# Kernel optimization log

Measured on AMD Instinct MI355X. Metric: run time of the kernel, lower is better.

## Reference

```python
import jax, jax.numpy as jnp
import numpy as np

DIM = 4096
N_HEADS = 32
HEAD_DIM = DIM // N_HEADS  # 128
BSZ = 2
SEQLEN = 2048


def setup_inputs() -> dict:
    key = jax.random.key(0)
    ks = jax.random.split(key, 8)
    x = jax.random.normal(ks[0], (BSZ, SEQLEN, DIM), dtype=jnp.float32)
    # rotary frequencies (LLaMA): theta = 10000^{-2i/d}, angle = pos * theta
    inv_freq = 1.0 / (10000.0 ** (np.arange(0, HEAD_DIM, 2, dtype=np.float32) / HEAD_DIM))
    angles = np.arange(SEQLEN, dtype=np.float32)[:, None] * inv_freq[None, :]  # [S, hd/2]
    freqs_cos = jnp.asarray(np.cos(angles))
    freqs_sin = jnp.asarray(np.sin(angles))
    # causal additive mask [1,1,S,S]
    neg = jnp.float32(-1e9)
    mask = jnp.where(jnp.tril(jnp.ones((SEQLEN, SEQLEN), dtype=bool)), 0.0, neg)[None, None]
    scale = 0.02
    wq = jax.random.normal(ks[1], (DIM, DIM), dtype=jnp.float32) * scale
    wk = jax.random.normal(ks[2], (DIM, DIM), dtype=jnp.float32) * scale
    wv = jax.random.normal(ks[3], (DIM, DIM), dtype=jnp.float32) * scale
    wo = jax.random.normal(ks[4], (DIM, DIM), dtype=jnp.float32) * scale
    return {"x": x, "start_pos": 0, "freqs_cos": freqs_cos, "freqs_sin": freqs_sin,
            "mask": mask, "wq": wq, "wk": wk, "wv": wv, "wo": wo}


def _apply_rotary(t, cos, sin):
    # t: [B,S,H,hd]; cos/sin: [S,hd/2] -> broadcast [1,S,1,hd/2]
    t = t.reshape(*t.shape[:-1], HEAD_DIM // 2, 2)
    t0, t1 = t[..., 0], t[..., 1]
    c = cos[None, :, None, :]
    s = sin[None, :, None, :]
    r0 = t0 * c - t1 * s
    r1 = t0 * s + t1 * c
    return jnp.stack([r0, r1], axis=-1).reshape(*t0.shape[:-1], HEAD_DIM)


def reference(x, start_pos, freqs_cos, freqs_sin, mask, wq, wk, wv, wo):
    bsz, seqlen, _ = x.shape
    # QKV projections (nn.Linear: y = x @ W.T; weights stored [out,in])
    xq = (x @ wq.T).reshape(bsz, seqlen, N_HEADS, HEAD_DIM)
    xk = (x @ wk.T).reshape(bsz, seqlen, N_HEADS, HEAD_DIM)
    xv = (x @ wv.T).reshape(bsz, seqlen, N_HEADS, HEAD_DIM)
    xq = _apply_rotary(xq, freqs_cos, freqs_sin)
    xk = _apply_rotary(xk, freqs_cos, freqs_sin)
    # [B,H,S,hd]
    q = xq.transpose(0, 2, 1, 3)
    k = xk.transpose(0, 2, 1, 3)
    v = xv.transpose(0, 2, 1, 3)
    scale = 1.0 / jnp.sqrt(jnp.float32(HEAD_DIM))
    scores = jnp.einsum('bhqd,bhkd->bhqk', q, k) * scale + mask
    probs = jax.nn.softmax(scores, axis=-1)
    out = jnp.einsum('bhqk,bhkd->bhqd', probs, v)  # [B,H,S,hd]
    out = out.transpose(0, 2, 1, 3).reshape(bsz, seqlen, DIM)
    return out @ wo.T
```

## Files before the change

kernel.cpp:

```cpp
#include <hip/hip_runtime.h>

typedef unsigned short ushort_t;
typedef unsigned int u32;
typedef short bf16x8 __attribute__((ext_vector_type(8)));
typedef float f32x4 __attribute__((ext_vector_type(4)));
typedef float f32x16 __attribute__((ext_vector_type(16)));
typedef u32 u32x4 __attribute__((ext_vector_type(4)));

__device__ __forceinline__ ushort_t f2bf(float f) {
  u32 u = __builtin_bit_cast(u32, f);
  u += 0x7FFFu + ((u >> 16) & 1u);
  return (ushort_t)(u >> 16);
}
__device__ __forceinline__ float bf2f(u32 bits16) {
  return __builtin_bit_cast(float, bits16 << 16);
}

__global__ __launch_bounds__(256)
void cvt_kernel(const float* __restrict__ in, ushort_t* __restrict__ out) {
  const int i = blockIdx.x * 256 + threadIdx.x;
  const float4 a = ((const float4*)in)[(size_t)i * 2];
  const float4 b = ((const float4*)in)[(size_t)i * 2 + 1];
  uint4 r;
  r.x = (u32)f2bf(a.x) | ((u32)f2bf(a.y) << 16);
  r.y = (u32)f2bf(a.z) | ((u32)f2bf(a.w) << 16);
  r.z = (u32)f2bf(b.x) | ((u32)f2bf(b.y) << 16);
  r.w = (u32)f2bf(b.z) | ((u32)f2bf(b.w) << 16);
  ((uint4*)out)[i] = r;
}

template <int F32OUT>
__global__ __launch_bounds__(512, 2)
void gemm256(const ushort_t* __restrict__ A, const ushort_t* __restrict__ B,
             void* __restrict__ C) {
  constexpr int KD = 4096, ND = 4096;
  __shared__ ushort_t sA[2][2][128 * 64];
  __shared__ ushort_t sB[2][2][128 * 64];
  const int tid = threadIdx.x;
  const int lane = tid & 63, wave = tid >> 6;
  const int lq = lane & 15, g = lane >> 4;
  const int wm = wave >> 2, wn = wave & 3;
  const int id = blockIdx.x;
  const int swz = (id & 7) * 32 + (id >> 3);
  const int bm = (swz >> 4) * 256;
  const int bn = (swz & 15) * 256;
  const int csw = ((lane & 7) ^ (lane >> 3)) * 8;
  const int srow = lane >> 3;

  f32x4 acc[8][4];
#pragma unroll
  for (int m = 0; m < 8; ++m)
#pragma unroll
    for (int n = 0; n < 4; ++n) acc[m][n] = (f32x4)0.f;

#define STG(sbuf, G, rowb, t_, s_, h_)                                               \
  {                                                                                  \
    _Pragma("unroll") for (int i_ = 0; i_ < 2; ++i_) {                               \
      const int r0_ = wave * 16 + i_ * 8;                                            \
      const int tc_ = (t_) > 63 ? 63 : (t_);                                         \
      const ushort_t* src_ =                                                         \
          (G) + (size_t)((rowb) + (h_) * 128 + r0_ + srow) * KD + tc_ * 64 + csw;    \
      __builtin_amdgcn_global_load_lds(                                              \
          (const __attribute__((address_space(1))) u32*)src_,                        \
          (__attribute__((address_space(3))) u32*)&sbuf[s_][h_][r0_ * 64 + lane * 8],\
          16, 0, 0);                                                                 \
    }                                                                                \
  }
#define LGKM0                                          \
  asm volatile("s_waitcnt lgkmcnt(0)" ::: "memory");   \
  __builtin_amdgcn_sched_barrier(0)

  STG(sA, A, bm, 0, 0, 0); STG(sA, A, bm, 0, 0, 1);
  STG(sB, B, bn, 0, 0, 0); STG(sB, B, bn, 0, 0, 1);
  asm volatile("s_waitcnt vmcnt(4)" ::: "memory");
  STG(sA, A, bm, 1, 1, 0); STG(sA, A, bm, 1, 1, 1);
  STG(sB, B, bn, 1, 1, 1);
  asm volatile("s_waitcnt vmcnt(6)" ::: "memory");
  __builtin_amdgcn_s_barrier();

  bf16x8 af[4][2], b0[2][2], b1[2][2];

  for (int t = 0; t < 64; ++t) {
    const int s = t & 1;
#pragma unroll
    for (int mf = 0; mf < 4; ++mf)
#pragma unroll
      for (int kk = 0; kk < 2; ++kk)
        af[mf][kk] = *(const bf16x8*)
            &sA[s][0][(wm * 64 + mf * 16 + lq) * 64 + (((kk * 4 + g) ^ (lq & 7)) * 8)];
#pragma unroll
    for (int nf = 0; nf < 2; ++nf)
#pragma unroll
      for (int kk = 0; kk < 2; ++kk)
        b0[nf][kk] = *(const bf16x8*)
            &sB[s][0][(wn * 32 + nf * 16 + lq) * 64 + (((kk * 4 + g) ^ (lq & 7)) * 8)];
    STG(sB, B, bn, t + 1, s ^ 1, 0);
    __builtin_amdgcn_s_barrier();
    LGKM0;
    __builtin_amdgcn_s_setprio(1);
#pragma unroll
    for (int mf = 0; mf < 4; ++mf)
#pragma unroll
      for (int nf = 0; nf < 2; ++nf)
#pragma unroll
        for (int kk = 0; kk < 2; ++kk)
          acc[mf][nf] = __builtin_amdgcn_mfma_f32_16x16x32_bf16(af[mf][kk], b0[nf][kk],
                                                                acc[mf][nf], 0, 0, 0);
    __builtin_amdgcn_s_setprio(0);
    __builtin_amdgcn_s_barrier();
#pragma unroll
    for (int nf = 0; nf < 2; ++nf)
#pragma unroll
      for (int kk = 0; kk < 2; ++kk)
        b1[nf][kk] = *(const bf16x8*)
            &sB[s][1][(wn * 32 + nf * 16 + lq) * 64 + (((kk * 4 + g) ^ (lq & 7)) * 8)];
    __builtin_amdgcn_s_barrier();
    LGKM0;
    __builtin_amdgcn_s_setprio(1);
#pragma unroll
    for (int mf = 0; mf < 4; ++mf)
#pragma unroll
      for (int nf = 0; nf < 2; ++nf)
#pragma unroll
        for (int kk = 0; kk < 2; ++kk)
          acc[mf][2 + nf] = __builtin_amdgcn_mfma_f32_16x16x32_bf16(af[mf][kk], b1[nf][kk],
                                                                    acc[mf][2 + nf], 0, 0, 0);
    __builtin_amdgcn_s_setprio(0);
    __builtin_amdgcn_s_barrier();
#pragma unroll
    for (int mf = 0; mf < 4; ++mf)
#pragma unroll
      for (int kk = 0; kk < 2; ++kk)
        af[mf][kk] = *(const bf16x8*)
            &sA[s][1][(wm * 64 + mf * 16 + lq) * 64 + (((kk * 4 + g) ^ (lq & 7)) * 8)];
    STG(sA, A, bm, t + 2, s, 0);
    __builtin_amdgcn_s_barrier();
    LGKM0;
    __builtin_amdgcn_s_setprio(1);
#pragma unroll
    for (int mf = 0; mf < 4; ++mf)
#pragma unroll
      for (int nf = 0; nf < 2; ++nf)
#pragma unroll
        for (int kk = 0; kk < 2; ++kk)
          acc[4 + mf][2 + nf] = __builtin_amdgcn_mfma_f32_16x16x32_bf16(
              af[mf][kk], b1[nf][kk], acc[4 + mf][2 + nf], 0, 0, 0);
    __builtin_amdgcn_s_setprio(0);
    __builtin_amdgcn_s_barrier();
    STG(sA, A, bm, t + 2, s, 1);
    STG(sB, B, bn, t + 2, s, 1);
    __builtin_amdgcn_s_barrier();
    __builtin_amdgcn_s_setprio(1);
#pragma unroll
    for (int mf = 0; mf < 4; ++mf)
#pragma unroll
      for (int nf = 0; nf < 2; ++nf)
#pragma unroll
        for (int kk = 0; kk < 2; ++kk)
          acc[4 + mf][nf] = __builtin_amdgcn_mfma_f32_16x16x32_bf16(
              af[mf][kk], b0[nf][kk], acc[4 + mf][nf], 0, 0, 0);
    __builtin_amdgcn_s_setprio(0);
    asm volatile("s_waitcnt vmcnt(6)" ::: "memory");
    __builtin_amdgcn_s_barrier();
  }
#undef STG
#undef LGKM0

#pragma unroll
  for (int m = 0; m < 8; ++m) {
    const int grow = bm + (m >> 2) * 128 + wm * 64 + (m & 3) * 16 + g * 4;
#pragma unroll
    for (int r = 0; r < 4; ++r)
#pragma unroll
      for (int n = 0; n < 4; ++n) {
        const int gcol = bn + (n >> 1) * 128 + wn * 32 + (n & 1) * 16 + lq;
        if (F32OUT)
          ((float*)C)[(size_t)(grow + r) * ND + gcol] = acc[m][n][r];
        else
          ((ushort_t*)C)[(size_t)(grow + r) * ND + gcol] = f2bf(acc[m][n][r]);
      }
  }
}

__global__ __launch_bounds__(256)
void rope_kernel(ushort_t* __restrict__ Q, ushort_t* __restrict__ K,
                 const float* __restrict__ fcos, const float* __restrict__ fsin) {
  const int gid = blockIdx.x * 256 + threadIdx.x;
  ushort_t* T = blockIdx.y ? K : Q;
  const float scale = blockIdx.y ? 1.f : 0.08838834764831845f;
  const int j8 = gid & 15;
  const int h = (gid >> 4) & 31;
  const int s = (gid >> 9) & 2047;
  const int b = gid >> 20;
  const size_t off = (size_t)(b * 2048 + s) * 4096 + h * 128 + j8 * 8;
  uint4 v = *(const uint4*)(T + off);
  const float4 c4 = *(const float4*)(fcos + s * 64 + j8 * 4);
  const float4 s4 = *(const float4*)(fsin + s * 64 + j8 * 4);
  u32 w[4] = {v.x, v.y, v.z, v.w};
  const float cc[4] = {c4.x, c4.y, c4.z, c4.w};
  const float ss[4] = {s4.x, s4.y, s4.z, s4.w};
#pragma unroll
  for (int p = 0; p < 4; ++p) {
    const float t0 = bf2f(w[p] & 0xffffu);
    const float t1 = bf2f(w[p] >> 16);
    const float r0 = (t0 * cc[p] - t1 * ss[p]) * scale;
    const float r1 = (t0 * ss[p] + t1 * cc[p]) * scale;
    w[p] = (u32)f2bf(r0) | ((u32)f2bf(r1) << 16);
  }
  v.x = w[0]; v.y = w[1]; v.z = w[2]; v.w = w[3];
  *(uint4*)(T + off) = v;
}

__global__ __launch_bounds__(256, 2)
void attn_kernel(const ushort_t* __restrict__ Q, const ushort_t* __restrict__ K,
                 const ushort_t* __restrict__ Vt, ushort_t* __restrict__ O) {
  __shared__ ushort_t sK[2][32 * 128];
  __shared__ ushort_t sV[2][128 * 32];
  __shared__ float sScr[4][32];

  const int lane = threadIdx.x & 63, wave = threadIdx.x >> 6;
  const int lq = lane & 31, hi = lane >> 5;
  const int bp = blockIdx.x;
  const int bh = bp >> 3, j = bp & 7;
  const int h = bh & 31, b = bh >> 5;
  const ushort_t* Kb_ = K + (size_t)(b * 2048) * 4096 + h * 128;
  const ushort_t* Vb_ = Vt + (size_t)(h * 128) * 4096 + b * 2048;

#define STAGE(buf, kt_)                                                              \
  {                                                                                  \
    const int kb_ = (kt_) * 32;                                                      \
    _Pragma("unroll")                                                                \
    for (int i_ = 0; i_ < 2; ++i_) {                                                 \
      const int c_ = wave + i_ * 4;                                                  \
      const int krow = c_ * 4 + (lane >> 4);                                         \
      const int kcol = (lane & 15) ^ (krow & 7);                                     \
      const ushort_t* ksrc = Kb_ + (size_t)(kb_ + krow) * 4096 + kcol * 8;           \
      __builtin_amdgcn_global_load_lds(                                              \
          (const __attribute__((address_space(1))) u32*)ksrc,                        \
          (__attribute__((address_space(3))) u32*)&sK[buf][c_ * 512 + lane * 8],     \
          16, 0, 0);                                                                 \
      const int sst = c_ * 64 + lane;                                                \
      const int dv = sst >> 2;                                                       \
      const int gl = (sst & 3) ^ ((sst >> 3) & 3);                                   \
      const ushort_t* vsrc = Vb_ + (size_t)dv * 4096 + kb_ + gl * 8;                 \
      __builtin_amdgcn_global_load_lds(                                              \
          (const __attribute__((address_space(1))) u32*)vsrc,                        \
          (__attribute__((address_space(3))) u32*)&sV[buf][sst * 8], 16, 0, 0);      \
    }                                                                                \
  }

  for (int ph = 0; ph < 2; ++ph) {
    const int qj = ph ? (15 - j) : j;
    const int qbase = qj * 128 + wave * 32;
    const int ntw = qj * 4 + wave + 1;
    const int ntmax = qj * 4 + 4;

    bf16x8 aq[8];
    const ushort_t* qrow = Q + (size_t)(b * 2048 + qbase + lq) * 4096 + h * 128 + hi * 8;
#pragma unroll
    for (int kf = 0; kf < 8; ++kf) aq[kf] = *(const bf16x8*)(qrow + kf * 16);

    f32x16 o[4];
#pragma unroll
    for (int dt = 0; dt < 4; ++dt) o[dt] = (f32x16)0.f;
    float m_run = -1e30f, l_run = 0.f;

    int cur = 0;
    STAGE(0, 0);
    __syncthreads();

    for (int kt = 0; kt < ntmax; ++kt) {
      if (kt + 1 < ntmax) STAGE(cur ^ 1, kt + 1);
      if (kt < ntw) {
        const int kb = kt * 32;
        f32x16 st = (f32x16)0.f;
#pragma unroll
        for (int kf = 0; kf < 8; ++kf) {
          const bf16x8 kfrag =
              *(const bf16x8*)&sK[cur][lq * 128 + (((kf * 2 + hi) ^ (lq & 7)) * 8)];
          st = __builtin_amdgcn_mfma_f32_32x32x16_bf16(kfrag, aq[kf], st, 0, 0, 0);
        }
        if (kt == ntw - 1) {
          const int q = qbase + lq;
#pragma unroll
          for (int r = 0; r < 16; ++r) {
            const int key = kb + (r & 3) + 8 * (r >> 2) + 4 * hi;
            if (key > q) st[r] = -1e30f;
          }
        }
        float tm = st[0];
#pragma unroll
        for (int r = 1; r < 16; ++r) tm = fmaxf(tm, st[r]);
        tm = fmaxf(tm, __shfl_xor(tm, 32));
        if (!__all(tm <= m_run + 8.f)) {
          const float mnew = fmaxf(m_run, tm);
          const float corr = __expf(m_run - mnew);
          m_run = mnew;
          l_run *= corr;
          if (hi == 0) sScr[wave][lq] = corr;
          float fr[16];
#pragma unroll
          for (int r = 0; r < 16; ++r)
            fr[r] = sScr[wave][(r & 3) + 8 * (r >> 2) + 4 * hi];
#pragma unroll
          for (int dt = 0; dt < 4; ++dt)
#pragma unroll
            for (int r = 0; r < 16; ++r) o[dt][r] *= fr[r];
        }
        float rs = 0.f;
#pragma unroll
        for (int r = 0; r < 16; ++r) { st[r] = __expf(st[r] - m_run); rs += st[r]; }
        rs += __shfl_xor(rs, 32);
        l_run += rs;
        u32 A_, B_, C_, D_, E_, F_, G_, H_;
#define CVTPK(d_, l_, h_) \
  asm("v_cvt_pk_bf16_f32 %0, %1, %2" : "=v"(d_) : "v"(l_), "v"(h_))
        CVTPK(A_, st[0], st[1]);  CVTPK(B_, st[4], st[5]);
        CVTPK(C_, st[2], st[3]);  CVTPK(D_, st[6], st[7]);
        CVTPK(E_, st[8], st[9]);  CVTPK(F_, st[12], st[13]);
        CVTPK(G_, st[10], st[11]); CVTPK(H_, st[14], st[15]);
#undef CVTPK
        asm volatile("v_permlane32_swap_b32 %0, %1" : "+v"(A_), "+v"(B_));
        asm volatile("v_permlane32_swap_b32 %0, %1" : "+v"(C_), "+v"(D_));
        asm volatile("v_permlane32_swap_b32 %0, %1" : "+v"(E_), "+v"(F_));
        asm volatile("v_permlane32_swap_b32 %0, %1" : "+v"(G_), "+v"(H_));
        const bf16x8 pa0 = __builtin_bit_cast(bf16x8, (u32x4){A_, C_, B_, D_});
        const bf16x8 pa1 = __builtin_bit_cast(bf16x8, (u32x4){E_, G_, F_, H_});
#pragma unroll
        for (int dt = 0; dt < 4; ++dt) {
          const int d0 = dt * 32 + lq;
          const int s0 = 4 * d0 + ((hi + 0) ^ ((d0 >> 1) & 3));
          const int s1 = 4 * d0 + ((hi + 2) ^ ((d0 >> 1) & 3));
          const bf16x8 vf0 = *(const bf16x8*)&sV[cur][s0 * 8];
          const bf16x8 vf1 = *(const bf16x8*)&sV[cur][s1 * 8];
          o[dt] = __builtin_amdgcn_mfma_f32_32x32x16_bf16(pa0, vf0, o[dt], 0, 0, 0);
          o[dt] = __builtin_amdgcn_mfma_f32_32x32x16_bf16(pa1, vf1, o[dt], 0, 0, 0);
        }
      }
      __syncthreads();
      cur ^= 1;
    }

    if (hi == 0) sScr[wave][lq] = 1.f / l_run;
    __syncthreads();
    const size_t obase = (size_t)(b * 2048 + qbase) * 4096 + h * 128;
#pragma unroll
    for (int r = 0; r < 16; ++r) {
      const int qr = (r & 3) + 8 * (r >> 2) + 4 * hi;
      const float f = sScr[wave][qr];
#pragma unroll
      for (int dt = 0; dt < 4; ++dt)
        O[obase + (size_t)qr * 4096 + dt * 32 + lq] = f2bf(o[dt][r] * f);
    }
    __syncthreads();
  }
#undef STAGE
}

extern "C" void kernel_launch(void* const* d_in, const int* in_sizes, int n_in,
                              void* d_out, int out_size, void* d_ws, size_t ws_size,
                              hipStream_t stream) {
  const float* x = (const float*)d_in[0];
  const float* fcos = (const float*)d_in[2];
  const float* fsin = (const float*)d_in[3];
  const float* wq = (const float*)d_in[5];
  const float* wk = (const float*)d_in[6];
  const float* wv = (const float*)d_in[7];
  const float* wo = (const float*)d_in[8];
  float* out = (float*)d_out;
  char* ws = (char*)d_ws;
  const size_t MB32 = 33554432;
  ushort_t* xb = (ushort_t*)(ws);
  ushort_t* wb = (ushort_t*)(ws + MB32);
  ushort_t* Qb = (ushort_t*)(ws + 2 * MB32);
  ushort_t* Kb = (ushort_t*)(ws + 3 * MB32);
  ushort_t* Vt = (ushort_t*)(ws + 4 * MB32);
  ushort_t* Ob = xb;

  const dim3 cb(256);
  const dim3 cg(8192);
  const dim3 gb(512);
  const dim3 gg(256);

  hipLaunchKernelGGL(cvt_kernel, cg, cb, 0, stream, x, xb);
  hipLaunchKernelGGL(cvt_kernel, cg, cb, 0, stream, wq, wb);
  hipLaunchKernelGGL((gemm256<0>), gg, gb, 0, stream, xb, wb, (void*)Qb);
  hipLaunchKernelGGL(cvt_kernel, cg, cb, 0, stream, wk, wb);
  hipLaunchKernelGGL((gemm256<0>), gg, gb, 0, stream, xb, wb, (void*)Kb);
  hipLaunchKernelGGL(cvt_kernel, cg, cb, 0, stream, wv, wb);
  hipLaunchKernelGGL((gemm256<0>), gg, gb, 0, stream, wb, xb, (void*)Vt);
  hipLaunchKernelGGL(rope_kernel, dim3(8192, 2), cb, 0, stream, Qb, Kb, fcos, fsin);
  hipLaunchKernelGGL(attn_kernel, dim3(512), cb, 0, stream, Qb, Kb, Vt, Ob);
  hipLaunchKernelGGL(cvt_kernel, cg, cb, 0, stream, wo, wb);
  hipLaunchKernelGGL((gemm256<1>), gg, gb, 0, stream, Ob, wb, (void*)out);
}
```

Before: 680.3 us.

## Prefetch next tile's B0 fragments during last MFMA phase of GEMM loop

Restructures the GEMM main loop into a 2x-unrolled macro where the next K-tile's B half-0 LDS fragments are read at the end of the current tile's final MFMA phase. This double-buffers the b0 registers and moves the global-load wait ahead of the last compute phase, removing one LDS-read stall per iteration. The prologue drops an intermediate vmcnt wait. It increases register pressure and changes barrier ordering, which risks hazards on the shared buffers.

```diff
diff --git a/kernel.cpp b/kernel.cpp
--- a/kernel.cpp
+++ b/kernel.cpp
@@ -69,102 +69,89 @@
 #define LGKM0                                          \
   asm volatile("s_waitcnt lgkmcnt(0)" ::: "memory");   \
   __builtin_amdgcn_sched_barrier(0)
+#define RD_A(S_, H_, mf_, kk_)                                                        \
+  (*(const bf16x8*)&sA[S_][H_][(wm * 64 + (mf_) * 16 + lq) * 64 +                     \
+                               ((((kk_) * 4 + g) ^ (lq & 7)) * 8)])
+#define RD_B(S_, H_, nf_, kk_)                                                        \
+  (*(const bf16x8*)&sB[S_][H_][(wn * 32 + (nf_) * 16 + lq) * 64 +                     \
+                               ((((kk_) * 4 + g) ^ (lq & 7)) * 8)])
+#define MM(MB, NB, BR)                                                                \
+  _Pragma("unroll") for (int mf = 0; mf < 4; ++mf)                                    \
+    _Pragma("unroll") for (int nf = 0; nf < 2; ++nf)                                  \
+      _Pragma("unroll") for (int kk = 0; kk < 2; ++kk)                                \
+        acc[(MB) + mf][(NB) + nf] = __builtin_amdgcn_mfma_f32_16x16x32_bf16(          \
+            af[mf][kk], BR[nf][kk], acc[(MB) + mf][(NB) + nf], 0, 0, 0)
 
   STG(sA, A, bm, 0, 0, 0); STG(sA, A, bm, 0, 0, 1);
   STG(sB, B, bn, 0, 0, 0); STG(sB, B, bn, 0, 0, 1);
-  asm volatile("s_waitcnt vmcnt(4)" ::: "memory");
   STG(sA, A, bm, 1, 1, 0); STG(sA, A, bm, 1, 1, 1);
   STG(sB, B, bn, 1, 1, 1);
   asm volatile("s_waitcnt vmcnt(6)" ::: "memory");
   __builtin_amdgcn_s_barrier();
 
-  bf16x8 af[4][2], b0[2][2], b1[2][2];
-
-  for (int t = 0; t < 64; ++t) {
-    const int s = t & 1;
-#pragma unroll
-    for (int mf = 0; mf < 4; ++mf)
-#pragma unroll
-      for (int kk = 0; kk < 2; ++kk)
-        af[mf][kk] = *(const bf16x8*)
-            &sA[s][0][(wm * 64 + mf * 16 + lq) * 64 + (((kk * 4 + g) ^ (lq & 7)) * 8)];
-#pragma unroll
-    for (int nf = 0; nf < 2; ++nf)
-#pragma unroll
-      for (int kk = 0; kk < 2; ++kk)
-        b0[nf][kk] = *(const bf16x8*)
-            &sB[s][0][(wn * 32 + nf * 16 + lq) * 64 + (((kk * 4 + g) ^ (lq & 7)) * 8)];
-    STG(sB, B, bn, t + 1, s ^ 1, 0);
-    __builtin_amdgcn_s_barrier();
-    LGKM0;
-    __builtin_amdgcn_s_setprio(1);
-#pragma unroll
-    for (int mf = 0; mf < 4; ++mf)
-#pragma unroll
-      for (int nf = 0; nf < 2; ++nf)
-#pragma unroll
-        for (int kk = 0; kk < 2; ++kk)
-          acc[mf][nf] = __builtin_amdgcn_mfma_f32_16x16x32_bf16(af[mf][kk], b0[nf][kk],
-                                                                acc[mf][nf], 0, 0, 0);
-    __builtin_amdgcn_s_setprio(0);
-    __builtin_amdgcn_s_barrier();
-#pragma unroll
-    for (int nf = 0; nf < 2; ++nf)
-#pragma unroll
-      for (int kk = 0; kk < 2; ++kk)
-        b1[nf][kk] = *(const bf16x8*)
-            &sB[s][1][(wn * 32 + nf * 16 + lq) * 64 + (((kk * 4 + g) ^ (lq & 7)) * 8)];
-    __builtin_amdgcn_s_barrier();
-    LGKM0;
-    __builtin_amdgcn_s_setprio(1);
-#pragma unroll
-    for (int mf = 0; mf < 4; ++mf)
-#pragma unroll
-      for (int nf = 0; nf < 2; ++nf)
-#pragma unroll
-        for (int kk = 0; kk < 2; ++kk)
-          acc[mf][2 + nf] = __builtin_amdgcn_mfma_f32_16x16x32_bf16(af[mf][kk], b1[nf][kk],
-                                                                    acc[mf][2 + nf], 0, 0, 0);
-    __builtin_amdgcn_s_setprio(0);
-    __builtin_amdgcn_s_barrier();
-#pragma unroll
-    for (int mf = 0; mf < 4; ++mf)
-#pragma unroll
-      for (int kk = 0; kk < 2; ++kk)
-        af[mf][kk] = *(const bf16x8*)
-            &sA[s][1][(wm * 64 + mf * 16 + lq) * 64 + (((kk * 4 + g) ^ (lq & 7)) * 8)];
-    STG(sA, A, bm, t + 2, s, 0);
-    __builtin_amdgcn_s_barrier();
-    LGKM0;
-    __builtin_amdgcn_s_setprio(1);
-#pragma unroll
-    for (int mf = 0; mf < 4; ++mf)
-#pragma unroll
-      for (int nf = 0; nf < 2; ++nf)
-#pragma unroll
-        for (int kk = 0; kk < 2; ++kk)
-          acc[4 + mf][2 + nf] = __builtin_amdgcn_mfma_f32_16x16x32_bf16(
-              af[mf][kk], b1[nf][kk], acc[4 + mf][2 + nf], 0, 0, 0);
-    __builtin_amdgcn_s_setprio(0);
-    __builtin_amdgcn_s_barrier();
-    STG(sA, A, bm, t + 2, s, 1);
-    STG(sB, B, bn, t + 2, s, 1);
-    __builtin_amdgcn_s_barrier();
-    __builtin_amdgcn_s_setprio(1);
-#pragma unroll
-    for (int mf = 0; mf < 4; ++mf)
-#pragma unroll
-      for (int nf = 0; nf < 2; ++nf)
-#pragma unroll
-        for (int kk = 0; kk < 2; ++kk)
-          acc[4 + mf][nf] = __builtin_amdgcn_mfma_f32_16x16x32_bf16(
-              af[mf][kk], b0[nf][kk], acc[4 + mf][nf], 0, 0, 0);
-    __builtin_amdgcn_s_setprio(0);
-    asm volatile("s_waitcnt vmcnt(6)" ::: "memory");
-    __builtin_amdgcn_s_barrier();
-  }
+  bf16x8 af[4][2], b1[2][2], b0c[2][2], b0n[2][2];
+#pragma unroll
+  for (int nf = 0; nf < 2; ++nf)
+#pragma unroll
+    for (int kk = 0; kk < 2; ++kk) b0c[nf][kk] = RD_B(0, 0, nf, kk);
+
+#define TILE(S_, T_, B0C, B0N)                                                        \
+                                 \
+  _Pragma("unroll") for (int mf = 0; mf < 4; ++mf)                                    \
+    _Pragma("unroll") for (int kk = 0; kk < 2; ++kk)                                  \
+      af[mf][kk] = RD_A(S_, 0, mf, kk);                                               \
+  STG(sB, B, bn, (T_) + 1, (S_) ^ 1, 0);                                              \
+  __builtin_amdgcn_s_barrier();                                                       \
+  LGKM0;                                                                              \
+  __builtin_amdgcn_s_setprio(1);                                                      \
+  MM(0, 0, B0C);                                                                      \
+  __builtin_amdgcn_s_setprio(0);                                                      \
+  __builtin_amdgcn_s_barrier();                                                       \
+                                                \
+  _Pragma("unroll") for (int nf = 0; nf < 2; ++nf)                                    \
+    _Pragma("unroll") for (int kk = 0; kk < 2; ++kk)                                  \
+      b1[nf][kk] = RD_B(S_, 1, nf, kk);                                               \
+  __builtin_amdgcn_s_barrier();                                                       \
+  LGKM0;                                                                              \
+  __builtin_amdgcn_s_setprio(1);                                                      \
+  MM(0, 2, b1);                                                                       \
+  __builtin_amdgcn_s_setprio(0);                                                      \
+  __builtin_amdgcn_s_barrier();                                                       \
+                                 \
+  _Pragma("unroll") for (int mf = 0; mf < 4; ++mf)                                    \
+    _Pragma("unroll") for (int kk = 0; kk < 2; ++kk)                                  \
+      af[mf][kk] = RD_A(S_, 1, mf, kk);                                               \
+  STG(sA, A, bm, (T_) + 2, S_, 0);                                                    \
+  __builtin_amdgcn_s_barrier();                                                       \
+  LGKM0;                                                                              \
+  __builtin_amdgcn_s_setprio(1);                                                      \
+  MM(4, 2, b1);                                                                       \
+  __builtin_amdgcn_s_setprio(0);                                                      \
+  __builtin_amdgcn_s_barrier();                                                       \
+    \
+  STG(sA, A, bm, (T_) + 2, S_, 1);                                                    \
+  STG(sB, B, bn, (T_) + 2, S_, 1);                                                    \
+  asm volatile("s_waitcnt vmcnt(6)" ::: "memory");                                    \
+  __builtin_amdgcn_s_barrier();                                                       \
+  LGKM0;                                                                              \
+  __builtin_amdgcn_s_setprio(1);                                                      \
+  MM(4, 0, B0C);                                                                      \
+  __builtin_amdgcn_s_setprio(0);                                                      \
+  _Pragma("unroll") for (int nf = 0; nf < 2; ++nf)                                    \
+    _Pragma("unroll") for (int kk = 0; kk < 2; ++kk)                                  \
+      B0N[nf][kk] = RD_B((S_) ^ 1, 0, nf, kk);                                        \
+  __builtin_amdgcn_s_barrier();
+
+  for (int t = 0; t < 64; t += 2) {
+    TILE(0, t, b0c, b0n)
+    TILE(1, t + 1, b0n, b0c)
+  }
+#undef TILE
 #undef STG
 #undef LGKM0
+#undef RD_A
+#undef RD_B
+#undef MM
 
 #pragma unroll
   for (int m = 0; m < 8; ++m) {
```

After: 679.4 us. Within noise of the previous version (-0.1%).
